# Performance work log

Measured on AMD Instinct MI355X. Metric: run time of the kernel, lower is better.

## Reference

```python
import jax, jax.numpy as jnp
import numpy as np

B, S, D = 2, 2048, 2048
G, HPG = 4, 4            # n_groups, heads_per_group (n_heads=16)
DH = D // (G * HPG)      # head dim d_q = d_k = d_v = 128


def setup_inputs() -> dict:
    key = jax.random.key(0)
    ks = jax.random.split(key, 14)
    s = 1.0 / np.sqrt(D)
    inp = {
        "query": jax.random.normal(ks[0], (B, S, D), jnp.float32),
        "key":   jax.random.normal(ks[1], (B, S, D), jnp.float32),
        "value": jax.random.normal(ks[2], (B, S, D), jnp.float32),
        # per-group, per-head Q projections; per-group shared K, V
        "WQ": jax.random.normal(ks[3], (G, HPG, DH, D), jnp.float32) * s,
        "bQ": jax.random.normal(ks[4], (G, HPG, DH), jnp.float32) * 0.01,
        "WK": jax.random.normal(ks[5], (G, DH, D), jnp.float32) * s,
        "bK": jax.random.normal(ks[6], (G, DH), jnp.float32) * 0.01,
        "WV": jax.random.normal(ks[7], (G, DH, D), jnp.float32) * s,
        "bV": jax.random.normal(ks[8], (G, DH), jnp.float32) * 0.01,
        "WO": jax.random.normal(ks[9], (D, G * HPG * DH), jnp.float32) * s,
        "bO": jax.random.normal(ks[10], (D,), jnp.float32) * 0.01,
    }
    return inp


def reference(query, key, value, WQ, bQ, WK, bK, WV, bV, WO, bO):
    # q: [B, G, HPG, S, DH] — all per-head Q projections as one batched GEMM
    q = jnp.einsum('bsd,ghqd->bghsq', query, WQ) + bQ[None, :, :, None, :]
    # k, v: [B, G, S, DH] — one K/V per group (shared across heads in group)
    k = jnp.einsum('bsd,gkd->bgsk', key, WK) + bK[None, :, None, :]
    v = jnp.einsum('bsd,gvd->bgsv', value, WV) + bV[None, :, None, :]
    scale = 1.0 / jnp.sqrt(jnp.asarray(DH, q.dtype))
    # scores: [B, G, HPG, S_q, S_k]
    scores = jnp.einsum('bghsq,bgtq->bghst', q, k) * scale
    attn = jax.nn.softmax(scores, axis=-1)
    out = jnp.einsum('bghst,bgtv->bghsv', attn, v)   # [B, G, HPG, S, DH]
    # concat heads group-major, then transpose(1,2) + flatten like the torch code
    out = out.reshape(B, G * HPG, S, DH).transpose(0, 2, 1, 3).reshape(B, S, G * HPG * DH)
    return out @ WO.T + bO
```

## Files before the change

kernel.cpp:

```cpp
#include <hip/hip_runtime.h>
#include <cstdint>
#include <cstddef>


typedef __attribute__((ext_vector_type(8)))  __bf16 bf16x8;
typedef __attribute__((ext_vector_type(4)))  __bf16 bf16x4;
typedef __attribute__((ext_vector_type(4)))  float  f32x4;
typedef __attribute__((ext_vector_type(16))) float  f32x16;
typedef __attribute__((ext_vector_type(4)))  unsigned int u32x4;

#define GLD16(gp, lp) __builtin_amdgcn_global_load_lds(                         \
    (__attribute__((address_space(1))) void*)(size_t)(gp),                     \
    (__attribute__((address_space(3))) void*)(lp), 16, 0, 0)

#define PLSWAP(a, b) asm volatile("v_permlane32_swap_b32 %0, %1" : "+v"(a), "+v"(b))
#define EXP2F(x) __builtin_amdgcn_exp2f(x)

static __device__ __forceinline__ unsigned pack2bf(float a, float b) {
    unsigned short ua = __builtin_bit_cast(unsigned short, (__bf16)a);
    unsigned short ub = __builtin_bit_cast(unsigned short, (__bf16)b);
    return (unsigned)ua | ((unsigned)ub << 16);
}

struct F2BArgs {
    const float* src[7];
    __bf16* dst[7];
    long beg[8];
};
__global__ void f2b_multi(F2BArgs a) {
    const long total = a.beg[7];
    const long stride = (long)gridDim.x * blockDim.x;
    for (long i = (long)blockIdx.x * blockDim.x + threadIdx.x; i < total; i += stride) {
        int s = 0;
#pragma unroll
        for (int j = 1; j < 7; ++j) s += (i >= a.beg[j]);
        long off = i - a.beg[s];
        const float4* p = (const float4*)(a.src[s] + off * 8);
        float4 x = p[0], y = p[1];
        bf16x8 r;
        r[0] = (__bf16)x.x; r[1] = (__bf16)x.y; r[2] = (__bf16)x.z; r[3] = (__bf16)x.w;
        r[4] = (__bf16)y.x; r[5] = (__bf16)y.y; r[6] = (__bf16)y.z; r[7] = (__bf16)y.w;
        *(bf16x8*)(a.dst[s] + off * 8) = r;
    }
}

template <int OUTF32>
static __device__ __forceinline__
void gemm256_body(const __bf16* __restrict__ A, const __bf16* __restrict__ Bm,
                  const float* __restrict__ bias, float* __restrict__ Cf,
                  __bf16* __restrict__ Cb, int N, int K, int m0, int n0,
                  int biasrow, __bf16* As, __bf16* Bs) {
    const int tid = threadIdx.x, lane = tid & 63, wid = tid >> 6;
    const int g = lane >> 4, c = lane & 15;
    const int wr = wid >> 1, wc = wid & 1;
    const int nkt = K >> 6;

    const f32x4 z = {0.f, 0.f, 0.f, 0.f};
    f32x4 acc[4][4];
#pragma unroll
    for (int i = 0; i < 4; ++i)
#pragma unroll
        for (int j = 0; j < 4; ++j) acc[i][j] = z;

    auto stageA = [&](int b, int kt, int h) {
        if (kt >= nkt) return;
        const __bf16* src = A + (size_t)m0 * K + (size_t)kt * 64;
#pragma unroll
        for (int i = 0; i < 2; ++i) {
            int ci = h * 1024 + i * 512 + tid;
            int row = ci >> 3, chg = (ci & 7) ^ (row & 7);
            GLD16(src + (size_t)row * K + chg * 8, &As[b * 16384 + ci * 8]);
        }
    };
    auto stageB = [&](int b, int kt) {
        if (kt >= nkt) return;
        const __bf16* src = Bm + (size_t)n0 * K + (size_t)kt * 64;
#pragma unroll
        for (int i = 0; i < 2; ++i) {
            int ci = i * 512 + tid;
            int row = ci >> 3, chg = (ci & 7) ^ (row & 7);
            GLD16(src + (size_t)row * K + chg * 8, &Bs[b * 8192 + ci * 8]);
        }
    };

    stageA(0, 0, 0); stageA(0, 0, 1); stageB(0, 0);
    stageA(1, 1, 0); stageA(1, 1, 1); stageB(1, 1);
    asm volatile("s_waitcnt vmcnt(6)" ::: "memory");
    __builtin_amdgcn_sched_barrier(0);
    __builtin_amdgcn_s_barrier();

    int bd = 0;
    for (int kt = 0; kt < nkt; ++kt) {
        const int bs = (bd >= 1) ? bd - 1 : 2;
        bf16x8 af[4], bfr[4];
#pragma unroll
        for (int ph = 0; ph < 2; ++ph) {
#pragma unroll
            for (int mi = 0; mi < 4; ++mi) {
                int row = wr * 64 + mi * 16 + c;
                int ch = (ph * 4 + g) ^ (c & 7);
                af[mi] = *(const bf16x8*)&As[bd * 16384 + row * 64 + ch * 8];
            }
#pragma unroll
            for (int ni = 0; ni < 4; ++ni) {
                int row = wc * 64 + ni * 16 + c;
                int ch = (ph * 4 + g) ^ (c & 7);
                bfr[ni] = *(const bf16x8*)&Bs[bd * 8192 + row * 64 + ch * 8];
            }
            if (ph == 0) {
                stageA(bs, kt + 2, 0);
            } else {
                stageA(bs, kt + 2, 1);
                stageB(bs, kt + 2);
            }
            __builtin_amdgcn_s_barrier();
            asm volatile("s_waitcnt lgkmcnt(0)" ::: "memory");
            __builtin_amdgcn_sched_barrier(0);
            __builtin_amdgcn_s_setprio(1);
#pragma unroll
            for (int mi = 0; mi < 4; ++mi)
#pragma unroll
                for (int ni = 0; ni < 4; ++ni)
                    acc[mi][ni] = __builtin_amdgcn_mfma_f32_16x16x32_bf16(
                        af[mi], bfr[ni], acc[mi][ni], 0, 0, 0);
            __builtin_amdgcn_s_setprio(0);
            if (ph == 1) {
                if (kt >= nkt - 2) asm volatile("s_waitcnt vmcnt(0)" ::: "memory");
                else               asm volatile("s_waitcnt vmcnt(6)" ::: "memory");
                __builtin_amdgcn_sched_barrier(0);
            }
            __builtin_amdgcn_s_barrier();
        }
        bd = (bd >= 2) ? 0 : bd + 1;
    }

#pragma unroll
    for (int mi = 0; mi < 4; ++mi) {
#pragma unroll
        for (int ni = 0; ni < 4; ++ni) {
            int col = n0 + wc * 64 + ni * 16 + c;
            float bvc = biasrow ? 0.f : bias[col];
#pragma unroll
            for (int r = 0; r < 4; ++r) {
                int row = m0 + wr * 64 + mi * 16 + g * 4 + r;
                float v = acc[mi][ni][r] + (biasrow ? bias[row] : bvc);
                if (OUTF32) Cf[(size_t)row * N + col] = v;
                else        Cb[(size_t)row * N + col] = (__bf16)v;
            }
        }
    }
}

__global__ __launch_bounds__(512)
void gemm_proj(const __bf16* __restrict__ qb, const __bf16* __restrict__ wqb,
               const float* __restrict__ bQ, __bf16* __restrict__ qp,
               const __bf16* __restrict__ kb, const __bf16* __restrict__ wkb,
               const float* __restrict__ bK, __bf16* __restrict__ kp,
               const __bf16* __restrict__ wvb, const __bf16* __restrict__ vb,
               const float* __restrict__ bV, __bf16* __restrict__ vpT) {
    __shared__ __bf16 As[3 * 256 * 64];
    __shared__ __bf16 Bs[3 * 128 * 64];
    const int bid = blockIdx.x;
    const int swz = (bid & 7) * 48 + (bid >> 3);
    if (swz < 256) {
        int bx = swz & 15, by = swz >> 4;
        gemm256_body<0>(qb, wqb, bQ, nullptr, qp, 2048, 2048,
                        by * 256, bx * 128, 0, As, Bs);
    } else if (swz < 320) {
        int s = swz - 256;
        int bx = s & 3, by = s >> 2;
        gemm256_body<0>(kb, wkb, bK, nullptr, kp, 512, 2048,
                        by * 256, bx * 128, 0, As, Bs);
    } else {
        int s = swz - 320;
        int bx = s & 31, by = s >> 5;
        gemm256_body<0>(wvb, vb, bV, nullptr, vpT, 4096, 2048,
                        by * 256, bx * 128, 1, As, Bs);
    }
}

__global__ __launch_bounds__(512)
void gemm_out(const __bf16* __restrict__ A, const __bf16* __restrict__ Bm,
              const float* __restrict__ bias, float* __restrict__ Cf) {
    __shared__ __bf16 As[3 * 256 * 64];
    __shared__ __bf16 Bs[3 * 128 * 64];
    const int bid = blockIdx.x;
    const int swz = (bid & 7) * 32 + (bid >> 3);
    int bx = swz & 15, by = swz >> 4;
    gemm256_body<1>(A, Bm, bias, Cf, nullptr, 2048, 2048,
                    by * 256, bx * 128, 0, As, Bs);
}

__global__ __launch_bounds__(256)
void attn_kernel(const __bf16* __restrict__ Qw, const __bf16* __restrict__ Kw,
                 const __bf16* __restrict__ VTw, __bf16* __restrict__ Ow) {
    constexpr int S = 2048, DQ = 2048, DKV = 512, TOK = 4096;
    constexpr int nt = S / 32;
    const int bid = blockIdx.x;
    const int xcd = bid & 7, slot = bid >> 3;
    const int b = xcd >> 2, grp = xcd & 3;
    const int head = grp * 4 + (slot & 3);
    const int qblk = slot >> 2;
    const int t0 = slot & (nt - 1);
    const __bf16* Q   = Qw + (size_t)b * S * DQ + head * 128;
    const __bf16* Kp  = Kw + (size_t)b * S * DKV + grp * 128;
    const __bf16* VTp = VTw + (size_t)(grp * 128) * TOK + (size_t)b * S;
    __bf16* Op = Ow + (size_t)b * S * DQ + head * 128;

    __shared__ __bf16 Ks[3][32 * 128];
    __shared__ __bf16 Vs[3][128 * 32];

    const int tid = threadIdx.x, wid = tid >> 6, lane = tid & 63;
    const int ql = lane & 31, hi = lane >> 5;
    const int qrow = qblk * 128 + wid * 32 + ql;

    bf16x8 qf[8];
#pragma unroll
    for (int ks = 0; ks < 8; ++ks)
        qf[ks] = *(const bf16x8*)(Q + (size_t)qrow * DQ + ks * 16 + hi * 8);

    f32x16 o[4];
#pragma unroll
    for (int d = 0; d < 4; ++d)
#pragma unroll
        for (int r = 0; r < 16; ++r) o[d][r] = 0.f;
    float mprev = -1e30f, lsum = 0.f;
    constexpr float kexp = 0.08838834764831845f * 1.4426950408889634f;
    constexpr float THR = 8.0f / kexp;

    auto stage = [&](int buf, int t) {
#pragma unroll
        for (int i = 0; i < 2; ++i) {
            int ci = i * 256 + tid;
            int key = ci >> 4, ccl = ci & 15, ccg = ccl ^ (key & 15);
            GLD16(Kp + (size_t)(t * 32 + key) * DKV + ccg * 8, &Ks[buf][ci * 8]);
        }
#pragma unroll
        for (int i = 0; i < 2; ++i) {
            int ci = i * 256 + tid;
            int dh = ci >> 2, cl = ci & 3, cg = cl ^ ((dh >> 1) & 3);
            GLD16(VTp + (size_t)dh * TOK + t * 32 + cg * 8, &Vs[buf][ci * 8]);
        }
    };

    stage(0, t0);
    stage(1, (t0 + 1) & (nt - 1));
    asm volatile("s_waitcnt vmcnt(4)" ::: "memory");
    asm volatile("s_barrier" ::: "memory");

    int bc = 0;
    for (int i = 0; i < nt; ++i) {
        const int bs = (bc >= 1) ? bc - 1 : 2;
        if (i + 2 < nt) stage(bs, (t0 + i + 2) & (nt - 1));

        f32x16 sc;
#pragma unroll
        for (int r = 0; r < 16; ++r) sc[r] = 0.f;
        __builtin_amdgcn_s_setprio(1);
#pragma unroll
        for (int ks = 0; ks < 8; ++ks) {
            int chl = (ks * 2 + hi) ^ (ql & 15);
            bf16x8 kf = *(const bf16x8*)&Ks[bc][ql * 128 + chl * 8];
            sc = __builtin_amdgcn_mfma_f32_32x32x16_bf16(kf, qf[ks], sc, 0, 0, 0);
        }
        __builtin_amdgcn_s_setprio(0);

        float mo = sc[0];
#pragma unroll
        for (int r = 1; r < 16; ++r) mo = fmaxf(mo, sc[r]);
        mo = fmaxf(mo, __shfl_xor(mo, 32, 64));
        if (!__all(mo - mprev <= THR)) {
            float mn = fmaxf(mprev, mo);
            float ef = EXP2F((mprev - mn) * kexp);
            lsum *= ef;
#pragma unroll
            for (int d = 0; d < 4; ++d)
#pragma unroll
                for (int r = 0; r < 16; ++r) o[d][r] *= ef;
            mprev = mn;
        }
        float mnk = mprev * kexp;
        float rs = 0.f;
#pragma unroll
        for (int r = 0; r < 16; ++r) {
            float p = EXP2F(__builtin_fmaf(sc[r], kexp, -mnk));
            sc[r] = p;
            rs += p;
        }
        rs += __shfl_xor(rs, 32, 64);
        lsum += rs;

        unsigned pk[4][2];
#pragma unroll
        for (int rg = 0; rg < 4; ++rg) {
            pk[rg][0] = pack2bf(sc[rg * 4 + 0], sc[rg * 4 + 1]);
            pk[rg][1] = pack2bf(sc[rg * 4 + 2], sc[rg * 4 + 3]);
        }

        __builtin_amdgcn_s_setprio(1);
#pragma unroll
        for (int e = 0; e < 2; ++e) {
            unsigned a0 = pk[2 * e][0], b0 = pk[2 * e + 1][0];
            unsigned a1 = pk[2 * e][1], b1 = pk[2 * e + 1][1];
            PLSWAP(a0, b0);
            PLSWAP(a1, b1);
            u32x4 fw = {a0, a1, b0, b1};
            bf16x8 pf = __builtin_bit_cast(bf16x8, fw);
#pragma unroll
            for (int dht = 0; dht < 4; ++dht) {
                int dh = dht * 32 + ql;
                int chl = (e * 2 + hi) ^ ((dh >> 1) & 3);
                bf16x8 vf = *(const bf16x8*)&Vs[bc][dh * 32 + chl * 8];
                o[dht] = __builtin_amdgcn_mfma_f32_32x32x16_bf16(vf, pf, o[dht], 0, 0, 0);
            }
        }
        __builtin_amdgcn_s_setprio(0);

        if (i + 2 < nt) asm volatile("s_waitcnt vmcnt(4)" ::: "memory");
        else            asm volatile("s_waitcnt vmcnt(0)" ::: "memory");
        asm volatile("s_barrier" ::: "memory");
        bc = (bc >= 2) ? 0 : bc + 1;
    }

    float inv = 1.0f / lsum;
#pragma unroll
    for (int dht = 0; dht < 4; ++dht)
#pragma unroll
        for (int rg = 0; rg < 4; ++rg) {
            bf16x4 wv;
#pragma unroll
            for (int j = 0; j < 4; ++j) wv[j] = (__bf16)(o[dht][rg * 4 + j] * inv);
            int dh0 = dht * 32 + rg * 8 + hi * 4;
            *(bf16x4*)(Op + (size_t)qrow * DQ + dh0) = wv;
        }
}

extern "C" void kernel_launch(void* const* d_in, const int* in_sizes, int n_in,
                              void* d_out, int out_size, void* d_ws, size_t ws_size,
                              hipStream_t stream) {
    (void)in_sizes; (void)n_in; (void)out_size; (void)ws_size;
    const float* query = (const float*)d_in[0];
    const float* key   = (const float*)d_in[1];
    const float* value = (const float*)d_in[2];
    const float* WQ = (const float*)d_in[3];
    const float* bQ = (const float*)d_in[4];
    const float* WK = (const float*)d_in[5];
    const float* bK = (const float*)d_in[6];
    const float* WV = (const float*)d_in[7];
    const float* bV = (const float*)d_in[8];
    const float* WO = (const float*)d_in[9];
    const float* bO = (const float*)d_in[10];
    float* out = (float*)d_out;

    __bf16* w = (__bf16*)d_ws;
    __bf16* qb  = w; w += (size_t)4096 * 2048;
    __bf16* kb  = w; w += (size_t)4096 * 2048;
    __bf16* vb  = w; w += (size_t)4096 * 2048;
    __bf16* wqb = w; w += (size_t)2048 * 2048;
    __bf16* wkb = w; w += (size_t)512 * 2048;
    __bf16* wvb = w; w += (size_t)512 * 2048;
    __bf16* wob = w; w += (size_t)2048 * 2048;
    __bf16* qp  = w; w += (size_t)4096 * 2048;
    __bf16* kp  = w; w += (size_t)4096 * 512;
    __bf16* vpT = w; w += (size_t)512 * 4096;
    __bf16* ao  = w; w += (size_t)4096 * 2048;

    F2BArgs fa;
    fa.src[0] = query; fa.dst[0] = qb;
    fa.src[1] = key;   fa.dst[1] = kb;
    fa.src[2] = value; fa.dst[2] = vb;
    fa.src[3] = WQ;    fa.dst[3] = wqb;
    fa.src[4] = WK;    fa.dst[4] = wkb;
    fa.src[5] = WV;    fa.dst[5] = wvb;
    fa.src[6] = WO;    fa.dst[6] = wob;
    const long n8s[7] = {1048576, 1048576, 1048576, 524288, 131072, 131072, 524288};
    long acc = 0;
    for (int i = 0; i < 7; ++i) { fa.beg[i] = acc; acc += n8s[i]; }
    fa.beg[7] = acc;
    f2b_multi<<<2048, 256, 0, stream>>>(fa);

    gemm_proj<<<384, 512, 0, stream>>>(qb, wqb, bQ, qp,
                                       kb, wkb, bK, kp,
                                       wvb, vb, bV, vpT);

    attn_kernel<<<512, 256, 0, stream>>>(qp, kp, vpT, ao);

    gemm_out<<<256, 512, 0, stream>>>(ao, wob, bO, out);
}
```

Before: 252.4 us.

## Software-pipeline QK^T of the next tile with softmax and PV of the current

Splits the attention loop body into a QK^T stage and a softmax-plus-PV stage, then unrolls the loop by two with alternating score registers. The QK^T MFMAs for tile i+1 are now issued before the softmax and PV of tile i. This lets matrix work overlap the exp/max vector work. Waits are tightened to vmcnt(2), so only the K half of the next stage must have landed before the next QK^T. The cost is a second live 16-float score accumulator, which raises register pressure, and the unrolled loop assumes an even tile count.

```diff
diff --git a/kernel.cpp b/kernel.cpp
--- a/kernel.cpp
+++ b/kernel.cpp
@@ -228,43 +228,39 @@
     constexpr float kexp = 0.08838834764831845f * 1.4426950408889634f;
     constexpr float THR = 8.0f / kexp;
 
-    auto stage = [&](int buf, int t) {
+    auto stage = [&](int t) {
+        int buf = t % 3;
+        int ta = (t0 + t) & (nt - 1);
 #pragma unroll
         for (int i = 0; i < 2; ++i) {
             int ci = i * 256 + tid;
             int key = ci >> 4, ccl = ci & 15, ccg = ccl ^ (key & 15);
-            GLD16(Kp + (size_t)(t * 32 + key) * DKV + ccg * 8, &Ks[buf][ci * 8]);
+            GLD16(Kp + (size_t)(ta * 32 + key) * DKV + ccg * 8, &Ks[buf][ci * 8]);
         }
 #pragma unroll
         for (int i = 0; i < 2; ++i) {
             int ci = i * 256 + tid;
             int dh = ci >> 2, cl = ci & 3, cg = cl ^ ((dh >> 1) & 3);
-            GLD16(VTp + (size_t)dh * TOK + t * 32 + cg * 8, &Vs[buf][ci * 8]);
+            GLD16(VTp + (size_t)dh * TOK + ta * 32 + cg * 8, &Vs[buf][ci * 8]);
         }
     };
 
-    stage(0, t0);
-    stage(1, (t0 + 1) & (nt - 1));
-    asm volatile("s_waitcnt vmcnt(4)" ::: "memory");
-    asm volatile("s_barrier" ::: "memory");
-
-    int bc = 0;
-    for (int i = 0; i < nt; ++i) {
-        const int bs = (bc >= 1) ? bc - 1 : 2;
-        if (i + 2 < nt) stage(bs, (t0 + i + 2) & (nt - 1));
-
-        f32x16 sc;
-#pragma unroll
-        for (int r = 0; r < 16; ++r) sc[r] = 0.f;
+    auto qkt = [&](int t, f32x16& scn) {
+        const __bf16* kb = &Ks[t % 3][0];
+#pragma unroll
+        for (int r = 0; r < 16; ++r) scn[r] = 0.f;
         __builtin_amdgcn_s_setprio(1);
 #pragma unroll
         for (int ks = 0; ks < 8; ++ks) {
             int chl = (ks * 2 + hi) ^ (ql & 15);
-            bf16x8 kf = *(const bf16x8*)&Ks[bc][ql * 128 + chl * 8];
-            sc = __builtin_amdgcn_mfma_f32_32x32x16_bf16(kf, qf[ks], sc, 0, 0, 0);
+            bf16x8 kf = *(const bf16x8*)&kb[ql * 128 + chl * 8];
+            scn = __builtin_amdgcn_mfma_f32_32x32x16_bf16(kf, qf[ks], scn, 0, 0, 0);
         }
         __builtin_amdgcn_s_setprio(0);
-
+    };
+
+    auto smpv = [&](int t, f32x16& sc) {
+        const __bf16* vb = &Vs[t % 3][0];
         float mo = sc[0];
 #pragma unroll
         for (int r = 1; r < 16; ++r) mo = fmaxf(mo, sc[r]);
@@ -310,16 +306,34 @@
             for (int dht = 0; dht < 4; ++dht) {
                 int dh = dht * 32 + ql;
                 int chl = (e * 2 + hi) ^ ((dh >> 1) & 3);
-                bf16x8 vf = *(const bf16x8*)&Vs[bc][dh * 32 + chl * 8];
+                bf16x8 vf = *(const bf16x8*)&vb[dh * 32 + chl * 8];
                 o[dht] = __builtin_amdgcn_mfma_f32_32x32x16_bf16(vf, pf, o[dht], 0, 0, 0);
             }
         }
         __builtin_amdgcn_s_setprio(0);
-
-        if (i + 2 < nt) asm volatile("s_waitcnt vmcnt(4)" ::: "memory");
+    };
+
+    f32x16 scA, scB;
+    stage(0);
+    stage(1);
+    asm volatile("s_waitcnt vmcnt(2)" ::: "memory");
+    asm volatile("s_barrier" ::: "memory");
+    qkt(0, scA);
+
+    for (int i = 0; i < nt; i += 2) {
+        if (i + 2 < nt) stage(i + 2);
+        qkt(i + 1, scB);
+        smpv(i, scA);
+        if (i + 2 < nt) asm volatile("s_waitcnt vmcnt(2)" ::: "memory");
         else            asm volatile("s_waitcnt vmcnt(0)" ::: "memory");
         asm volatile("s_barrier" ::: "memory");
-        bc = (bc >= 2) ? 0 : bc + 1;
+
+        if (i + 3 < nt) stage(i + 3);
+        if (i + 2 < nt) qkt(i + 2, scA);
+        smpv(i + 1, scB);
+        if (i + 3 < nt) asm volatile("s_waitcnt vmcnt(2)" ::: "memory");
+        else            asm volatile("s_waitcnt vmcnt(0)" ::: "memory");
+        asm volatile("s_barrier" ::: "memory");
     }
 
     float inv = 1.0f / lsum;
```

After: 246.5 us, median of 3. -2.3%, faster.
